# Kernel optimization log

Measured on AMD Instinct MI355X. Metric: run time of the kernel, lower is better.

Reference implementation:

```python
import jax, jax.numpy as jnp
import numpy as np

N, C_IN, C_OUT, H, W_DIM = 8, 512, 512, 64, 512
K = 3              # conv_kernel
UP, DOWN = 2, 2    # up/down factors
TAPS = 12          # filter_size * factor
PAD = (9, 8, 9, 8) # px0, px1, py0, py1 from __init__ padding formula
GAIN = np.sqrt(2).astype(np.float32)
SLOPE = 0.2
CLAMP = 256.0


def _kaiser_beta(atten):
    if atten > 50:
        return 0.1102 * (atten - 8.7)
    if atten > 21:
        return 0.5842 * (atten - 21) ** 0.4 + 0.07886 * (atten - 21)
    return 0.0


def design_lowpass_filter(numtaps, cutoff, width, fs):
    # numpy re-implementation of scipy.signal.firwin (kaiser window, pass_zero, scale=True)
    nyq = fs / 2.0
    atten = 2.285 * (numtaps - 1) * np.pi * (width / nyq) + 7.95  # kaiser_atten
    beta = _kaiser_beta(atten)
    m = np.arange(numtaps) - (numtaps - 1) / 2.0
    c = cutoff / nyq
    h = c * np.sinc(c * m) * np.kaiser(numtaps, beta)
    h /= h.sum()
    return h.astype(np.float32)


def setup_inputs() -> dict:
    key = jax.random.key(0)
    ks = jax.random.split(key, 6)
    x = jax.random.normal(ks[0], (N, C_IN, H, H), dtype=jnp.float32)
    w = jax.random.normal(ks[1], (N, W_DIM), dtype=jnp.float32)
    affine_weight = jax.random.normal(ks[2], (C_IN, W_DIM), dtype=jnp.float32)
    affine_bias = jnp.ones((C_IN,), dtype=jnp.float32)  # bias_init=1
    conv_weight = jax.random.normal(ks[3], (C_OUT, C_IN, K, K), dtype=jnp.float32)
    conv_bias = jnp.zeros((C_OUT,), dtype=jnp.float32)
    up_filter = jnp.asarray(design_lowpass_filter(TAPS, cutoff=16.0, width=32.0, fs=128.0))
    down_filter = jnp.asarray(design_lowpass_filter(TAPS, cutoff=16.0, width=32.0, fs=128.0))
    magnitude_ema = jnp.ones((), dtype=jnp.float32)
    return {"x": x, "w": w, "affine_weight": affine_weight, "affine_bias": affine_bias,
            "conv_weight": conv_weight, "conv_bias": conv_bias,
            "up_filter": up_filter, "down_filter": down_filter,
            "magnitude_ema": magnitude_ema}


_DN = ('NCHW', 'OIHW', 'NCHW')


def upfirdn2d(x, f, up, down, pad, gain=1.0):
    # upsample (zero-insert) -> pad -> convolve with flipped separable filter -> downsample
    n, c, h, w = x.shape
    fr = jnp.flip(f).astype(x.dtype)
    kv = fr.reshape(1, 1, -1, 1)
    kh = fr.reshape(1, 1, 1, -1)
    y = x.reshape(n * c, 1, h, w)
    # +up-1 on the high side matches torch upfirdn2d's trailing zeros after upsampling
    y = jax.lax.conv_general_dilated(y, kv, (down, 1), ((pad[2], pad[3] + up - 1), (0, 0)),
                                     lhs_dilation=(up, 1), dimension_numbers=_DN)
    y = jax.lax.conv_general_dilated(y, kh, (1, down), ((0, 0), (pad[0], pad[1] + up - 1)),
                                     lhs_dilation=(1, up), dimension_numbers=_DN)
    return y.reshape(n, c, y.shape[2], y.shape[3]) * gain


def modulated_conv2d(x, w, s, input_gain, padding):
    # demodulate=True pre-normalization (StyleGAN3)
    w = w * jax.lax.rsqrt(jnp.mean(jnp.square(w), axis=(1, 2, 3), keepdims=True))
    s = s * jax.lax.rsqrt(jnp.mean(jnp.square(s)))
    wk = w[None] * s[:, None, :, None, None]                       # [N,O,I,k,k]
    d = jax.lax.rsqrt(jnp.sum(jnp.square(wk), axis=(2, 3, 4)) + 1e-8)  # [N,O]
    wk = wk * d[:, :, None, None, None] * input_gain

    def per_sample(xi, wi):
        return jax.lax.conv_general_dilated(xi[None], wi, (1, 1),
                                            ((padding, padding), (padding, padding)),
                                            dimension_numbers=_DN)[0]
    return jax.vmap(per_sample)(x, wk.astype(x.dtype))


def reference(x, w, affine_weight, affine_bias, conv_weight, conv_bias,
              up_filter, down_filter, magnitude_ema):
    # affine: FullyConnectedLayer with weight_gain = 1/sqrt(w_dim)
    styles = w @ affine_weight.T * (1.0 / np.sqrt(W_DIM)) + affine_bias
    input_gain = jax.lax.rsqrt(magnitude_ema)
    y = modulated_conv2d(x, conv_weight, styles, input_gain, padding=K - 1)  # [N,O,66,66]
    # filtered_lrelu: bias -> upsample FIR (gain=up^2) -> lrelu*sqrt(2), clamp -> downsample FIR
    y = y + conv_bias[None, :, None, None]
    y = upfirdn2d(y, up_filter, up=UP, down=1, pad=PAD, gain=float(UP) ** 2)
    y = jnp.where(y >= 0, y, SLOPE * y) * GAIN
    y = jnp.clip(y, -CLAMP, CLAMP)
    y = upfirdn2d(y, down_filter, up=1, down=DOWN, pad=(0, 0, 0, 0))  # [N,O,64,64]
    return y
```

## Files before the change

### kernel.cpp

```cpp
#include <hip/hip_runtime.h>
#include <cstdint>

#define DEV __device__ __forceinline__

static constexpr float INV_SQRT_W = 0.04419417382415922f;

typedef _Float16 half8 __attribute__((ext_vector_type(8)));
typedef float    f32x4 __attribute__((ext_vector_type(4)));

#define GLL16(g, l) __builtin_amdgcn_global_load_lds( \
    (const __attribute__((address_space(1))) void*)(g), \
    (__attribute__((address_space(3))) void*)(l), 16, 0, 0)

DEV int imax(int a, int b) { return a > b ? a : b; }
DEV int imin(int a, int b) { return a < b ? a : b; }

__global__ __launch_bounds__(256) void k_styles(const float* __restrict__ w,
    const float* __restrict__ aw, const float* __restrict__ ab,
    float* __restrict__ styles) {
  int t = blockIdx.x * 256 + threadIdx.x;
  int n = t >> 9, c = t & 511;
  const float* wr = w + n * 512;
  const float* ar = aw + c * 512;
  float s = 0.f;
  for (int k = 0; k < 512; ++k) s = fmaf(wr[k], ar[k], s);
  styles[t] = s * INV_SQRT_W + ab[c];
}

__global__ __launch_bounds__(256) void k_wstats(const float* __restrict__ cw,
    float* __restrict__ wsq, float* __restrict__ wscale) {
  int o = blockIdx.x;
  __shared__ float red[256];
  float tot = 0.f;
  for (int i = threadIdx.x; i < 512; i += 256) {
    const float* p = cw + (o * 512 + i) * 9;
    float s = 0.f;
#pragma unroll
    for (int k = 0; k < 9; ++k) s = fmaf(p[k], p[k], s);
    wsq[o * 512 + i] = s;
    tot += s;
  }
  red[threadIdx.x] = tot;
  __syncthreads();
  for (int st = 128; st > 0; st >>= 1) {
    if (threadIdx.x < st) red[threadIdx.x] += red[threadIdx.x + st];
    __syncthreads();
  }
  if (threadIdx.x == 0) wscale[o] = rsqrtf(red[0] / 4608.f);
}

__global__ __launch_bounds__(256) void k_sg(const float* __restrict__ styles,
                                            float* __restrict__ sg) {
  __shared__ float red[256];
  float s = 0.f;
  for (int t = threadIdx.x; t < 4096; t += 256) { float v = styles[t]; s = fmaf(v, v, s); }
  red[threadIdx.x] = s;
  __syncthreads();
  for (int st = 128; st > 0; st >>= 1) {
    if (threadIdx.x < st) red[threadIdx.x] += red[threadIdx.x + st];
    __syncthreads();
  }
  if (threadIdx.x == 0) sg[0] = rsqrtf(red[0] / 4096.f);
}

__global__ __launch_bounds__(256) void k_coef(const float* __restrict__ styles,
    const float* __restrict__ wsq, const float* __restrict__ wscale,
    const float* __restrict__ sg, const float* __restrict__ ema,
    float* __restrict__ coef) {
  int n = blockIdx.x >> 1;
  int o = ((blockIdx.x & 1) << 8) + threadIdx.x;
  __shared__ float s2[512];
  for (int i = threadIdx.x; i < 512; i += 256) { float v = styles[n * 512 + i]; s2[i] = v * v; }
  __syncthreads();
  const float* wq = wsq + o * 512;
  float Q = 0.f;
  for (int i = 0; i < 512; ++i) Q = fmaf(s2[i], wq[i], Q);
  float a = wscale[o] * sg[0];
  float ig = rsqrtf(ema[0]);
  coef[n * 512 + o] = ig * rsqrtf(a * a * Q + 1e-8f);
}

__global__ __launch_bounds__(256) void k_xprep(const float* __restrict__ x,
    const float* __restrict__ styles, const float* __restrict__ sg,
    _Float16* __restrict__ xT) {
  const int b = blockIdx.x;
  const int r = b & 63, ic = (b >> 6) & 15, n = b >> 10;
  const int tid = threadIdx.x;
  const int c = tid >> 2, s = tid & 3;
  const float sgv = sg[0];
  const int sig = ((r * 68 + c + 2) >> 1) & 3;
  const int i0 = ic * 32 + (s ^ sig) * 8;
  half8 v;
#pragma unroll
  for (int j = 0; j < 8; ++j) {
    int i = i0 + j;
    float xv = x[(((size_t)n * 512 + i) * 64 + r) * 64 + c];
    v[j] = (_Float16)(xv * styles[n * 512 + i] * sgv);
  }
  *(half8*)(xT + ((((size_t)(n * 16 + ic) * 64 + r) * 64 + c) * 32) + s * 8) = v;
}

__global__ __launch_bounds__(256) void k_wprep(const float* __restrict__ cw,
    const float* __restrict__ wscale, _Float16* __restrict__ w2) {
  int t = blockIdx.x * 256 + threadIdx.x;
  int s = t & 3;
  int o = (t >> 2) & 511;
  int ic = (t >> 11) & 15;
  int k9 = t >> 15;
  float wsc = wscale[o];
  half8 v;
#pragma unroll
  for (int j = 0; j < 8; ++j) {
    int i = ic * 32 + s * 8 + j;
    v[j] = (_Float16)(cw[((size_t)o * 512 + i) * 9 + k9] * wsc);
  }
  *(half8*)(w2 + (size_t)t * 8) = v;
}

__global__ __launch_bounds__(256, 3) void k_conv(
    const _Float16* __restrict__ xT, const _Float16* __restrict__ w2,
    const float* __restrict__ coef, _Float16* __restrict__ convpart) {
  const int b = blockIdx.x;
  const int kx = b & 7;
  const int j = b >> 3;
  const int ot = kx >> 1;
  const int n = (kx & 1) * 4 + j / 70;
  const int jj0 = j % 70;
  const int pt = jj0 >> 1;
  const int kh = jj0 & 1;
  const int p0 = pt * 128;
  const int R0 = p0 / 66;
  const int oBase = ot * 128;

  const int tid = threadIdx.x;
  const int wave = tid >> 6;
  const int lane = tid & 63;
  const int wo = wave >> 1, wp = wave & 1;
  const int isub = lane >> 4;
  const int l15 = lane & 15;

  __shared__ _Float16 patch[10880];

  int rloc[4], rr2[4], cc[4]; bool valid[4];
#pragma unroll
  for (int nt = 0; nt < 4; ++nt) {
    int p = p0 + wp * 64 + nt * 16 + l15;
    valid[nt] = (p < 4356);
    if (!valid[nt]) p = 4355;
    int r = p / 66;
    rloc[nt] = r - R0;
    rr2[nt] = r - 2;
    cc[nt] = p - r * 66;
  }

  f32x4 acc[4][4];
#pragma unroll
  for (int mt = 0; mt < 4; ++mt)
#pragma unroll
    for (int nt = 0; nt < 4; ++nt) acc[mt][nt] = (f32x4){0.f, 0.f, 0.f, 0.f};

  const int oA = oBase + wo * 64 + l15;
  const _Float16* wp0 = w2 + (size_t)oA * 32 + isub * 8;

  {
    _Float16* dst = &patch[0];
    if (tid < 80) {
      int pix = tid >> 2, s = tid & 3;
      int rl = pix >> 2, ci = pix & 3;
      int cl = (ci < 2) ? ci : (ci + 64);
      half8 z = {};
      *(half8*)(dst + (rl * 68 + cl) * 32 + s * 8) = z;
    }
#pragma unroll
    for (int rl = 0; rl < 5; ++rl) {
      int rin = R0 - 2 + rl;
      if (rin < 0 || rin >= 64) {
        for (int u = tid; u < 272; u += 256) {
          half8 z = {};
          *(half8*)(dst + rl * 68 * 32 + u * 8) = z;
        }
      }
    }
  }

  auto stage_rows = [&](int ic) {
    const _Float16* src = xT + ((size_t)(n * 16 + ic) * 4096) * 32;
    _Float16* dst = &patch[0];
#pragma unroll
    for (int rl = 0; rl < 5; ++rl) {
      int rin = R0 - 2 + rl;
      if (rin >= 0 && rin < 64)
        GLL16(src + (size_t)rin * 2048 + tid * 8, dst + (rl * 68 + 2) * 32 + tid * 8);
    }
  };

  auto LOADA = [&](half8 (&a)[4], int k9, int ic) {
#pragma unroll
    for (int mt = 0; mt < 4; ++mt)
      a[mt] = *(const half8*)(wp0 + ((size_t)(k9 * 16 + ic) * 512 + mt * 16) * 32);
  };
  auto STEP = [&](half8 (&a)[4], int k9) {
    const int dr = k9 / 3, dc = k9 % 3;
    const _Float16* pb = &patch[0];
#pragma unroll
    for (int nt = 0; nt < 4; ++nt) {
      int rl = rloc[nt] + dr;
      int cl = cc[nt] + dc;
      int sig = (((rr2[nt] + dr) * 68 + cl) >> 1) & 3;
      half8 bF = *(const half8*)(pb + (rl * 68 + cl) * 32 + ((isub ^ sig) << 3));
#pragma unroll
      for (int mt = 0; mt < 4; ++mt)
        acc[mt][nt] = __builtin_amdgcn_mfma_f32_16x16x32_f16(a[mt], bF, acc[mt][nt], 0, 0, 0);
    }
  };

  const int ic0 = kh * 8;
  stage_rows(ic0);
  __syncthreads();

  half8 aA[4], aB[4];
  for (int icl = 0; icl < 8; ++icl) {
    const int ic = ic0 + icl;

    LOADA(aA, 0, ic);
    LOADA(aB, 1, ic); STEP(aA, 0);
    LOADA(aA, 2, ic); STEP(aB, 1);
    LOADA(aB, 3, ic); STEP(aA, 2);
    LOADA(aA, 4, ic); STEP(aB, 3);
    LOADA(aB, 5, ic); STEP(aA, 4);
    LOADA(aA, 6, ic); STEP(aB, 5);
    LOADA(aB, 7, ic); STEP(aA, 6);
    LOADA(aA, 8, ic); STEP(aB, 7);
    STEP(aA, 8);

    __syncthreads();
    if (icl < 7) {
      stage_rows(ic + 1);
      __syncthreads();
    }
  }

  _Float16* outbase = convpart + (size_t)kh * 17842176;
#pragma unroll
  for (int mt = 0; mt < 4; ++mt) {
    const int o = oBase + wo * 64 + mt * 16 + isub * 4;
#pragma unroll
    for (int jj = 0; jj < 4; ++jj) {
      const float cf = coef[n * 512 + o + jj];
      _Float16* outp = outbase + (size_t)(n * 512 + o + jj) * 4356;
#pragma unroll
      for (int nt = 0; nt < 4; ++nt) {
        if (valid[nt]) {
          int p = p0 + wp * 64 + nt * 16 + l15;
          outp[p] = (_Float16)(acc[mt][nt][jj] * cf);
        }
      }
    }
  }
}

__global__ __launch_bounds__(256) void k_flrelu(const _Float16* __restrict__ convpart,
    const float* __restrict__ cbias, const float* __restrict__ fu,
    const float* __restrict__ fd, float* __restrict__ out) {
  const int img = blockIdx.x >> 2;
  const int tile = blockIdx.x & 3;
  const int P0 = tile * 16;
  const int c = img & 511;
  const int tid = threadIdx.x;

  __shared__ float As[26 * 68];
  __shared__ float Bs[42 * 76];
  __shared__ float Vs[42 * 64];

  float fupr[12], fdr[12];
#pragma unroll
  for (int jj = 0; jj < 12; ++jj) { fupr[jj] = fu[jj]; fdr[jj] = fd[11 - jj]; }

  {
    const _Float16* srcA = convpart + (size_t)img * 4356;
    const _Float16* srcB = srcA + 17842176;
    const float bias = cbias[c];
    for (int t = tid; t < 26 * 68; t += 256) {
      int r = t / 68, cc2 = t - r * 68;
      int gr = P0 - 4 + r;
      float v = 0.f;
      if (cc2 < 66 && gr >= 0 && gr < 66) {
        int idx = gr * 66 + cc2;
        v = (float)srcA[idx] + (float)srcB[idx] + bias;
      }
      As[t] = v;
    }
  }
  __syncthreads();

  for (int t = tid; t < 42 * 33; t += 256) {
    int kk2 = t / 33, m2 = t - kk2 * 33;
    int e = kk2 & 1, kk = (kk2 - e) >> 1;
    const float* Ab = &As[kk * 68 + 2 * m2];
    float sx = 0.f, sy = 0.f;
#pragma unroll
    for (int jj = 0; jj < 6; ++jj) {
      float2 a = *(const float2*)(Ab + (5 - jj) * 68);
      float f = e ? fupr[2 * jj + 1] : fupr[2 * jj];
      sx = fmaf(f, a.x, sx);
      sy = fmaf(f, a.y, sy);
    }
    float2 s2v = make_float2(sx, sy);
    *(float2*)&Bs[kk2 * 76 + 4 + 2 * m2] = s2v;
  }
  for (int t = tid; t < 42 * 10; t += 256) {
    int kk2 = t / 10, ci = t - kk2 * 10;
    int col = (ci < 4) ? ci : (66 + ci);
    Bs[kk2 * 76 + col] = 0.f;
  }
  __syncthreads();

  float* Us = As;
  for (int kc = 0; kc < 4; ++kc) {
    const int k0 = kc * 12;
    const int nrows = imin(42 - k0, 12);
    for (int t = tid; t < nrows * 70; t += 256) {
      int kr = t / 70, m = t - kr * 70;
      const float* Bk = &Bs[(k0 + kr) * 76];
      float ue = 0.f, uo = 0.f;
#pragma unroll
      for (int jj = 0; jj < 6; ++jj) {
        float bb = Bk[m + 5 - jj];
        ue = fmaf(fupr[2 * jj], bb, ue);
        uo = fmaf(fupr[2 * jj + 1], bb, uo);
      }
      ue *= (ue >= 0.f) ? 5.65685424949238f : 1.13137084989848f;
      uo *= (uo >= 0.f) ? 5.65685424949238f : 1.13137084989848f;
      ue = fminf(256.f, fmaxf(-256.f, ue));
      uo = fminf(256.f, fmaxf(-256.f, uo));
      *(float2*)&Us[kr * 140 + 2 * m] = make_float2(ue, uo);
    }
    __syncthreads();
    for (int t = tid; t < nrows * 64; t += 256) {
      int kr = t >> 6, q = t & 63;
      const float* Ur = &Us[kr * 140 + 2 * q];
      float v = 0.f;
#pragma unroll
      for (int jj = 0; jj < 12; ++jj) v = fmaf(fdr[jj], Ur[jj], v);
      Vs[(k0 + kr) * 64 + q] = v;
    }
    __syncthreads();
  }

  for (int t = tid; t < 1024; t += 256) {
    int pr = t >> 6, q = t & 63;
    const float* Vb = &Vs[2 * pr * 64 + q];
    float s = 0.f;
#pragma unroll
    for (int jj = 0; jj < 12; ++jj) s = fmaf(fdr[jj], Vb[jj * 64], s);
    out[(size_t)img * 4096 + (P0 + pr) * 64 + q] = s;
  }
}

extern "C" void kernel_launch(void* const* d_in, const int* in_sizes, int n_in,
                              void* d_out, int out_size, void* d_ws, size_t ws_size,
                              hipStream_t stream) {
  const float* x   = (const float*)d_in[0];
  const float* w   = (const float*)d_in[1];
  const float* aw  = (const float*)d_in[2];
  const float* ab  = (const float*)d_in[3];
  const float* cw  = (const float*)d_in[4];
  const float* cb  = (const float*)d_in[5];
  const float* fu  = (const float*)d_in[6];
  const float* fd  = (const float*)d_in[7];
  const float* ema = (const float*)d_in[8];
  float* out = (float*)d_out;

  float* ws       = (float*)d_ws;
  float* styles   = ws;
  float* wsq      = styles + 4096;
  float* wscale   = wsq + 262144;
  float* coef     = wscale + 512;
  float* sg       = coef + 4096;
  _Float16* convpart = (_Float16*)(sg + 8);
  _Float16* xT    = convpart + 35684352;
  _Float16* w2    = xT + 16777216;

  k_styles<<<16, 256, 0, stream>>>(w, aw, ab, styles);
  k_sg<<<1, 256, 0, stream>>>(styles, sg);
  k_wstats<<<512, 256, 0, stream>>>(cw, wsq, wscale);
  k_coef<<<16, 256, 0, stream>>>(styles, wsq, wscale, sg, ema, coef);
  k_xprep<<<8192, 256, 0, stream>>>(x, styles, sg, xT);
  k_wprep<<<1152, 256, 0, stream>>>(cw, wscale, w2);
  k_conv<<<2240, 256, 0, stream>>>(xT, w2, coef, convpart);
  k_flrelu<<<16384, 256, 0, stream>>>(convpart, cb, fu, fd, out);
}
```

Before: 406.8 us.

## Double-buffer LDS input patch and deepen weight prefetch in modulated conv

Doubles the shared-memory input patch so the next channel group's rows are staged with async global-to-LDS loads while the current group is computed. This removes one of the two barriers per iteration. Weight-fragment prefetch goes from two to three register buffers. All B fragments are loaded before each MFMA burst, which runs at raised wave priority. LDS use doubles to about 43 KB per block, which may lower occupancy, and extra registers are needed.

```diff
diff --git a/kernel.cpp b/kernel.cpp
--- a/kernel.cpp
+++ b/kernel.cpp
@@ -139,7 +139,7 @@
   const int isub = lane >> 4;
   const int l15 = lane & 15;
 
-  __shared__ _Float16 patch[10880];
+  __shared__ _Float16 patch[2][10880];
 
   int rloc[4], rr2[4], cc[4]; bool valid[4];
 #pragma unroll
@@ -162,8 +162,9 @@
   const int oA = oBase + wo * 64 + l15;
   const _Float16* wp0 = w2 + (size_t)oA * 32 + isub * 8;
 
-  {
-    _Float16* dst = &patch[0];
+#pragma unroll
+  for (int buf = 0; buf < 2; ++buf) {
+    _Float16* dst = &patch[buf][0];
     if (tid < 80) {
       int pix = tid >> 2, s = tid & 3;
       int rl = pix >> 2, ci = pix & 3;
@@ -183,9 +184,9 @@
     }
   }
 
-  auto stage_rows = [&](int ic) {
+  auto stage_rows = [&](int ic, int buf) {
     const _Float16* src = xT + ((size_t)(n * 16 + ic) * 4096) * 32;
-    _Float16* dst = &patch[0];
+    _Float16* dst = &patch[buf][0];
 #pragma unroll
     for (int rl = 0; rl < 5; ++rl) {
       int rin = R0 - 2 + rl;
@@ -199,45 +200,49 @@
     for (int mt = 0; mt < 4; ++mt)
       a[mt] = *(const half8*)(wp0 + ((size_t)(k9 * 16 + ic) * 512 + mt * 16) * 32);
   };
-  auto STEP = [&](half8 (&a)[4], int k9) {
+  auto STEP = [&](half8 (&a)[4], int k9, const _Float16* pb) {
     const int dr = k9 / 3, dc = k9 % 3;
-    const _Float16* pb = &patch[0];
+    half8 bF[4];
 #pragma unroll
     for (int nt = 0; nt < 4; ++nt) {
       int rl = rloc[nt] + dr;
       int cl = cc[nt] + dc;
       int sig = (((rr2[nt] + dr) * 68 + cl) >> 1) & 3;
-      half8 bF = *(const half8*)(pb + (rl * 68 + cl) * 32 + ((isub ^ sig) << 3));
+      bF[nt] = *(const half8*)(pb + (rl * 68 + cl) * 32 + ((isub ^ sig) << 3));
+    }
+    __builtin_amdgcn_s_setprio(1);
+#pragma unroll
+    for (int nt = 0; nt < 4; ++nt)
 #pragma unroll
       for (int mt = 0; mt < 4; ++mt)
-        acc[mt][nt] = __builtin_amdgcn_mfma_f32_16x16x32_f16(a[mt], bF, acc[mt][nt], 0, 0, 0);
-    }
+        acc[mt][nt] = __builtin_amdgcn_mfma_f32_16x16x32_f16(a[mt], bF[nt], acc[mt][nt], 0, 0, 0);
+    __builtin_amdgcn_s_setprio(0);
   };
 
   const int ic0 = kh * 8;
-  stage_rows(ic0);
-  __syncthreads();
-
-  half8 aA[4], aB[4];
+  stage_rows(ic0, 0);
+  __syncthreads();
+
+  half8 aA[4], aB[4], aC[4];
   for (int icl = 0; icl < 8; ++icl) {
     const int ic = ic0 + icl;
-
-    LOADA(aA, 0, ic);
-    LOADA(aB, 1, ic); STEP(aA, 0);
-    LOADA(aA, 2, ic); STEP(aB, 1);
-    LOADA(aB, 3, ic); STEP(aA, 2);
-    LOADA(aA, 4, ic); STEP(aB, 3);
-    LOADA(aB, 5, ic); STEP(aA, 4);
-    LOADA(aA, 6, ic); STEP(aB, 5);
-    LOADA(aB, 7, ic); STEP(aA, 6);
-    LOADA(aA, 8, ic); STEP(aB, 7);
-    STEP(aA, 8);
-
-    __syncthreads();
-    if (icl < 7) {
-      stage_rows(ic + 1);
-      __syncthreads();
-    }
+    const int buf = icl & 1;
+    const _Float16* pb = &patch[buf][0];
+
+    LOADA(aA, 0, ic); LOADA(aB, 1, ic); LOADA(aC, 2, ic);
+    if (icl < 7) stage_rows(ic + 1, buf ^ 1);
+
+    STEP(aA, 0, pb); LOADA(aA, 3, ic);
+    STEP(aB, 1, pb); LOADA(aB, 4, ic);
+    STEP(aC, 2, pb); LOADA(aC, 5, ic);
+    STEP(aA, 3, pb); LOADA(aA, 6, ic);
+    STEP(aB, 4, pb); LOADA(aB, 7, ic);
+    STEP(aC, 5, pb); LOADA(aC, 8, ic);
+    STEP(aA, 6, pb);
+    STEP(aB, 7, pb);
+    STEP(aC, 8, pb);
+
+    __syncthreads();
   }
 
   _Float16* outbase = convpart + (size_t)kh * 17842176;
```

Result: slower. 523.8 us (+28.7%).
